# Optimization experiments

Measured on AMD Instinct MI355X. Metric: run time of the kernel, lower is better.

Reference implementation:

```python
import jax, jax.numpy as jnp
import numpy as np

DN = ('NCHW', 'OIHW', 'NCHW')
B, T, D, H, W = 8, 10, 10, 128, 128
WINDOW_OUT = 5


def conv2d(x, w, b):
    y = jax.lax.conv_general_dilated(x, w, (1, 1), 'SAME', dimension_numbers=DN)
    return y + b[None, :, None, None]


def lstm_cell(x, h, c, w, b):
    # ConvLSTM gate update: conv over [x; h], split into i,f,o,g
    z = conv2d(jnp.concatenate([x, h], axis=1), w, b)
    i, f, o, g = jnp.split(z, 4, axis=1)
    c2 = jax.nn.sigmoid(f) * c + jax.nn.sigmoid(i) * jnp.tanh(g)
    h2 = jax.nn.sigmoid(o) * jnp.tanh(c2)
    return h2, c2


def attn_score(x, h, c, w1, b1, w2, b2):
    # conv-MLP attention score over concat([x, h, c]) -> (b, H, W)
    z = jnp.concatenate([x, h, c], axis=1)
    return conv2d(jnp.tanh(conv2d(z, w1, b1)), w2, b2)[:, 0]


def setup_inputs():
    key = jax.random.key(0)
    ks = jax.random.split(key, 16)
    s = 0.05
    return {
        'x': jax.random.normal(ks[0], (B, T, D, H, W), jnp.float32),
        'h0': jnp.zeros((B, 1, H, W), jnp.float32),
        'c0': jnp.zeros((B, 1, H, W), jnp.float32),
        'h1': jnp.zeros((B, 64, H, W), jnp.float32),
        'c1': jnp.zeros((B, 64, H, W), jnp.float32),
        # encoder cells: layer0 (in 10, hid 1), layer1 (in 1, hid 64)
        'w_enc0': jax.random.normal(ks[1], (4, 11, 3, 3), jnp.float32) * s,
        'b_enc0': jax.random.normal(ks[2], (4,), jnp.float32) * s,
        'w_enc1': jax.random.normal(ks[3], (256, 65, 3, 3), jnp.float32) * s,
        'b_enc1': jax.random.normal(ks[4], (256,), jnp.float32) * s,
        # decoder cells: layer0 (in 1, hid 64), layer1 (in 64, hid 1)
        'w_dec0': jax.random.normal(ks[5], (256, 65, 3, 3), jnp.float32) * s,
        'b_dec0': jax.random.normal(ks[6], (256,), jnp.float32) * s,
        'w_dec1': jax.random.normal(ks[7], (4, 65, 3, 3), jnp.float32) * s,
        'b_dec1': jax.random.normal(ks[8], (4,), jnp.float32) * s,
        # input attention: in 10+2*1=12 -> 32 -> 1
        'wa1': jax.random.normal(ks[9], (32, 12, 3, 3), jnp.float32) * s,
        'ba1': jax.random.normal(ks[10], (32,), jnp.float32) * s,
        'wa2': jax.random.normal(ks[11], (1, 32, 3, 3), jnp.float32) * s,
        'ba2': jax.random.normal(ks[12], (1,), jnp.float32) * s,
        # temporal attention: in 1+2*64=129 -> 32 -> 1
        'wt1': jax.random.normal(ks[13], (32, 129, 3, 3), jnp.float32) * s,
        'bt1': jax.random.normal(ks[14], (32,), jnp.float32) * s,
        'wt2': jax.random.normal(ks[15], (1, 32, 3, 3), jnp.float32) * s,
        'bt2': jnp.zeros((1,), jnp.float32),
    }


def reference(x, h0, c0, h1, c1, w_enc0, b_enc0, w_enc1, b_enc1,
              w_dec0, b_dec0, w_dec1, b_dec1,
              wa1, ba1, wa2, ba2, wt1, bt1, wt2, bt2):
    def input_attn(xx, h, c):
        # per-feature score; vmap over feature dim k (axis 2 of x)
        score = jax.vmap(lambda xk: attn_score(xk, h, c, wa1, ba1, wa2, ba2),
                         in_axes=2, out_axes=1)(xx)          # (b, D, H, W)
        alpha = jax.nn.softmax(score, axis=1)
        return xx * alpha[:, None]                            # broadcast over time

    # ---- encoder layer 0: input attention re-weights x every step (compounding)
    def step0(carry, t):
        xx, h, c = carry
        xx = input_attn(xx, h, c)
        h, c = lstm_cell(xx[:, t], h, c, w_enc0, b_enc0)
        return (xx, h, c), (h, c)

    _, (hs0, cs0) = jax.lax.scan(step0, (x, h0, c0), jnp.arange(T))
    hs0 = jnp.moveaxis(hs0, 0, 1)   # (b, T, 1, H, W)
    cs0 = jnp.moveaxis(cs0, 0, 1)

    # ---- encoder layer 1
    def step1(carry, xt):
        h, c = lstm_cell(xt, carry[0], carry[1], w_enc1, b_enc1)
        return (h, c), (h, c)

    _, (hs1, cs1) = jax.lax.scan(step1, (h1, c1), jnp.moveaxis(hs0, 1, 0))
    hs1 = jnp.moveaxis(hs1, 0, 1)   # (b, T, 64, H, W)
    cs1 = jnp.moveaxis(cs1, 0, 1)

    def temporal_attn(y, hb, cb):
        score = jax.vmap(lambda ht, ct: attn_score(y, ht, ct, wt1, bt1, wt2, bt2),
                         in_axes=1, out_axes=1)(hb, cb)       # (b, T, H, W)
        beta = jax.nn.softmax(score, axis=1)
        return jnp.sum(hb * beta[:, :, None], axis=1), cb[:, -1]

    # ---- decoder: states reversed -> layer0 uses encoder layer1 states, etc.
    y0 = x[:, -1, 0][:, None]       # x[:, [-1], selected_dim] -> (b, 1, H, W)

    def dec_step(carry, _):
        y, hb0, cb0, hb1, cb1 = carry
        ht, ct = temporal_attn(y, hb0, cb0)
        ht, ct = lstm_cell(y, ht, ct, w_dec0, b_dec0)
        y = ht
        hb0 = jnp.concatenate([hb0[:, 1:], ht[:, None]], axis=1)
        cb0 = jnp.concatenate([cb0[:, 1:], ct[:, None]], axis=1)
        ht2, ct2 = lstm_cell(y, hb1[:, -1], cb1[:, -1], w_dec1, b_dec1)
        y = ht2
        hb1 = jnp.concatenate([hb1[:, 1:], ht2[:, None]], axis=1)
        cb1 = jnp.concatenate([cb1[:, 1:], ct2[:, None]], axis=1)
        return (y, hb0, cb0, hb1, cb1), y

    _, ys = jax.lax.scan(dec_step, (y0, hs1, cs1, hs0, cs0), None, length=WINDOW_OUT)
    return jnp.moveaxis(ys, 0, 1)   # (b, window_out, 1, H, W)
```

## Files before the change

kernel.cpp:

```cpp
#include <hip/hip_runtime.h>


#define PX 16384L
#define T_ 10
#define D_ 10

__device__ __forceinline__ float fast_tanh(float x) {
    const float e = __builtin_exp2f(x * 2.88539008f);
    return 1.f - 2.f * __builtin_amdgcn_rcpf(e + 1.f);
}
__device__ __forceinline__ float fast_sig(float x) {
    const float e = __builtin_exp2f(x * -1.44269504f);
    return __builtin_amdgcn_rcpf(e + 1.f);
}
__device__ __forceinline__ float fast_exp(float x) {
    return __builtin_exp2f(x * 1.44269504f);
}

__device__ __forceinline__ void lstm_dev(
    float* lds,
    int tile, int hcb, int b,
    const float* __restrict__ in0, long bs0,
    const float* __restrict__ in1,
    const float* __restrict__ w, const float* __restrict__ bias,
    const float* __restrict__ cprev,
    float* __restrict__ hout, float* __restrict__ cout_)
{
    const int tid = threadIdx.x;
    const int tx = tid & 31, r0 = (tid >> 5) << 1;
    const int tileX = (tile & 3) << 5, tileY = (tile >> 2) << 4;
    const int hc0 = hcb << 1;
    float acc[16];
#pragma unroll
    for (int j = 0; j < 16; j++) acc[j] = 0.f;

    int g0[3]; float m0[3];
#pragma unroll
    for (int i = 0; i < 3; i++) {
        const int lidx = tid + i * 256;
        const int r = lidx / 34, cc = lidx - r * 34;
        const int gy = tileY + r - 1, gx = tileX + cc - 1;
        const bool inb = (lidx < 612) && ((unsigned)gy < 128u) && ((unsigned)gx < 128u);
        g0[i] = inb ? gy * 128 + gx : 0;
        m0[i] = inb ? 1.f : 0.f;
    }

    for (int cb = 0; cb < 65; cb += 8) {
        const int cmax = min(8, 65 - cb);
        for (int cl = 0; cl < cmax; cl++) {
            const int ci = cb + cl;
            const float* p = (ci == 0) ? in0 + (long)b * bs0
                                       : in1 + ((long)b * 64 + (ci - 1)) * PX;
#pragma unroll
            for (int i = 0; i < 3; i++) {
                const int lidx = tid + i * 256;
                if (lidx < 612) lds[cl * 612 + lidx] = m0[i] * p[g0[i]];
            }
        }
        __syncthreads();
        for (int cl = 0; cl < cmax; cl++) {
            float win[4][3];
#pragma unroll
            for (int dy = 0; dy < 4; dy++)
#pragma unroll
                for (int dx = 0; dx < 3; dx++)
                    win[dy][dx] = lds[cl * 612 + (r0 + dy) * 34 + tx + dx];
            const int ci = cb + cl;
#pragma unroll
            for (int j = 0; j < 2; j++)
#pragma unroll
                for (int g = 0; g < 4; g++) {
                    const float* wp = w + ((long)(g * 64 + hc0 + j) * 65 + ci) * 9;
#pragma unroll
                    for (int rr = 0; rr < 2; rr++) {
                        float a = acc[(j * 4 + g) * 2 + rr];
#pragma unroll
                        for (int ky = 0; ky < 3; ky++)
#pragma unroll
                            for (int kx = 0; kx < 3; kx++)
                                a = fmaf(wp[ky * 3 + kx], win[rr + ky][kx], a);
                        acc[(j * 4 + g) * 2 + rr] = a;
                    }
                }
        }
        __syncthreads();
    }
#pragma unroll
    for (int j = 0; j < 2; j++) {
        const int hc = hc0 + j;
        const float bi = bias[hc], bf = bias[64 + hc];
        const float bo = bias[128 + hc], bg = bias[192 + hc];
#pragma unroll
        for (int rr = 0; rr < 2; rr++) {
            const long opix = (long)(tileY + r0 + rr) * 128 + tileX + tx;
            const float i_ = fast_sig(acc[(j * 4 + 0) * 2 + rr] + bi);
            const float f_ = fast_sig(acc[(j * 4 + 1) * 2 + rr] + bf);
            const float o_ = fast_sig(acc[(j * 4 + 2) * 2 + rr] + bo);
            const float g_ = fast_tanh(acc[(j * 4 + 3) * 2 + rr] + bg);
            const float cp = cprev[((long)b * 64 + hc) * PX + opix];
            const float c2 = f_ * cp + i_ * g_;
            const float h2 = o_ * fast_tanh(c2);
            hout[((long)b * 64 + hc) * PX + opix] = h2;
            cout_[((long)b * 64 + hc) * PX + opix] = c2;
        }
    }
}

__device__ __forceinline__ void zpart_dev(
    float* lds,
    int tile, int cob, int b,
    const float* __restrict__ hsrc, const float* __restrict__ csrc,
    const float* __restrict__ wt1, const float* __restrict__ bt1,
    float* __restrict__ zdst)
{
    const int tid = threadIdx.x;
    const int tx = tid & 15, ty = tid >> 4;
    const int tileX = (tile & 7) << 4, tileY = (tile >> 3) << 4;
    const int co0 = cob << 3;
    float acc[8];
#pragma unroll
    for (int j = 0; j < 8; j++) acc[j] = 0.f;

    int g0[2]; float m0[2];
#pragma unroll
    for (int i = 0; i < 2; i++) {
        const int lidx = tid + i * 256;
        const int r = lidx / 18, cc = lidx - r * 18;
        const int gy = tileY + r - 1, gx = tileX + cc - 1;
        const bool inb = (lidx < 324) && ((unsigned)gy < 128u) && ((unsigned)gx < 128u);
        g0[i] = inb ? gy * 128 + gx : 0;
        m0[i] = inb ? 1.f : 0.f;
    }

    for (int cb = 0; cb < 128; cb += 4) {
        for (int cl = 0; cl < 4; cl++) {
            const int ci = cb + cl;
            const float* p = (ci < 64) ? hsrc + ((long)b * 64 + ci) * PX
                                       : csrc + ((long)b * 64 + (ci - 64)) * PX;
#pragma unroll
            for (int i = 0; i < 2; i++) {
                const int lidx = tid + i * 256;
                if (lidx < 324) lds[cl * 324 + lidx] = m0[i] * p[g0[i]];
            }
        }
        __syncthreads();
        for (int cl = 0; cl < 4; cl++) {
            float r9[9];
#pragma unroll
            for (int dy = 0; dy < 3; dy++)
#pragma unroll
                for (int dx = 0; dx < 3; dx++)
                    r9[dy * 3 + dx] = lds[cl * 324 + (ty + dy) * 18 + tx + dx];
            const int ci = cb + cl;
#pragma unroll
            for (int j = 0; j < 8; j++) {
                const float* wp = wt1 + ((long)(co0 + j) * 129 + 1 + ci) * 9;
                float a = acc[j];
#pragma unroll
                for (int q = 0; q < 9; q++) a = fmaf(wp[q], r9[q], a);
                acc[j] = a;
            }
        }
        __syncthreads();
    }
    const long opix = (long)(tileY + ty) * 128 + tileX + tx;
#pragma unroll
    for (int j = 0; j < 8; j++)
        zdst[((long)b * 32 + co0 + j) * PX + opix] = acc[j] + bt1[co0 + j];
}

__global__ __launch_bounds__(256)
void lstm_merge_k(const float* __restrict__ in0, long bs0,
                  const float* __restrict__ in1,
                  const float* __restrict__ w, const float* __restrict__ bias,
                  const float* __restrict__ cprev,
                  float* __restrict__ hout, float* __restrict__ cout_,
                  const float* __restrict__ zh, const float* __restrict__ zc,
                  float* __restrict__ zdst,
                  const float* __restrict__ wt1, const float* __restrict__ bt1)
{
    __shared__ float lds[8 * 612];
    const int bid = blockIdx.x, b = blockIdx.z;
    if (bid < 1024) {
        lstm_dev(lds, bid & 31, bid >> 5, b, in0, bs0, in1, w, bias,
                 cprev, hout, cout_);
    } else {
        const int q = bid - 1024;
        zpart_dev(lds, q & 63, q >> 6, b, zh, zc, wt1, bt1, zdst);
    }
}

__global__ __launch_bounds__(256)
void zpart_k(const float* __restrict__ zh, const float* __restrict__ zc,
             float* __restrict__ zdst,
             const float* __restrict__ wt1, const float* __restrict__ bt1)
{
    __shared__ float lds[4 * 324];
    zpart_dev(lds, blockIdx.x, blockIdx.y, blockIdx.z, zh, zc, wt1, bt1, zdst);
}

__global__ __launch_bounds__(256)
void dec_merge_k(const float* __restrict__ hs1s,
                 const float* __restrict__ hb1, long hb1bs,
                 const float* __restrict__ w1,
                 float* __restrict__ l1p, int nbs,
                 const float* __restrict__ zc, float* __restrict__ zdst,
                 const float* __restrict__ wt1, const float* __restrict__ bt1)
{
    __shared__ float lds[4 * 324];
    const int bid = blockIdx.x, b = blockIdx.z;
    if (bid < 256) {
        const int tile = bid & 63, s = bid >> 6;
        const int ci0 = (s == 0) ? 0 : (s == 1) ? 17 : (s == 2) ? 33 : 49;
        const int cn  = (s == 0) ? 17 : 16;
        const int tid = threadIdx.x;
        const int tx = tid & 15, ty = tid >> 4;
        const int tileX = (tile & 7) << 4, tileY = (tile >> 3) << 4;
        int g0[2]; float m0[2];
#pragma unroll
        for (int i = 0; i < 2; i++) {
            const int lidx = tid + i * 256;
            const int r = lidx / 18, cc = lidx - r * 18;
            const int gy = tileY + r - 1, gx = tileX + cc - 1;
            const bool inb = (lidx < 324) && ((unsigned)gy < 128u) && ((unsigned)gx < 128u);
            g0[i] = inb ? gy * 128 + gx : 0;
            m0[i] = inb ? 1.f : 0.f;
        }
        float acc[4] = {0.f, 0.f, 0.f, 0.f};
        for (int cb = 0; cb < cn; cb += 4) {
            const int cmax = min(4, cn - cb);
            for (int cl = 0; cl < cmax; cl++) {
                const int ci = ci0 + cb + cl;
                const float* p = (ci < 64) ? hs1s + ((long)b * 64 + ci) * PX
                                           : hb1 + (long)b * hb1bs;
#pragma unroll
                for (int i = 0; i < 2; i++) {
                    const int lidx = tid + i * 256;
                    if (lidx < 324) lds[cl * 324 + lidx] = m0[i] * p[g0[i]];
                }
            }
            __syncthreads();
            for (int cl = 0; cl < cmax; cl++) {
                float r9[9];
#pragma unroll
                for (int dy = 0; dy < 3; dy++)
#pragma unroll
                    for (int dx = 0; dx < 3; dx++)
                        r9[dy * 3 + dx] = lds[cl * 324 + (ty + dy) * 18 + tx + dx];
                const int ci = ci0 + cb + cl;
#pragma unroll
                for (int j = 0; j < 4; j++) {
                    const float* wp = w1 + ((long)j * 65 + ci) * 9;
                    float a = acc[j];
#pragma unroll
                    for (int q = 0; q < 9; q++) a = fmaf(wp[q], r9[q], a);
                    acc[j] = a;
                }
            }
            __syncthreads();
        }
        const long opix = (long)(tileY + ty) * 128 + tileX + tx;
#pragma unroll
        for (int j = 0; j < 4; j++)
            l1p[(((long)s * nbs + b) * 4 + j) * PX + opix] = acc[j];
    } else {
        const int q = bid - 256;
        zpart_dev(lds, q & 63, q >> 6, b, hs1s, zc, wt1, bt1, zdst);
    }
}

__global__ __launch_bounds__(256)
void combine_lstm_k(const float* __restrict__ pbuf, int nsl, int hidden,
                    const float* __restrict__ bias,
                    const float* __restrict__ cprev, long cpbs,
                    float* __restrict__ hout, long hobs,
                    float* __restrict__ cout_, long cobs,
                    float* __restrict__ hout2, long ho2bs, int rb, int nbs)
{
    const long idx = (long)blockIdx.x * 256 + threadIdx.x;
    if (idx >= (long)rb * hidden * PX) return;
    const long px = idx & 16383;
    const long v = idx >> 14;
    const int hc = (int)(v % hidden), b = (int)(v / hidden);
    const int nco = 4 * hidden;
    float g4[4] = {0.f, 0.f, 0.f, 0.f};
    for (int s = 0; s < nsl; s++)
#pragma unroll
        for (int g = 0; g < 4; g++)
            g4[g] += pbuf[(((long)s * nbs + b) * nco + g * hidden + hc) * PX + px];
    const float i_ = fast_sig(g4[0] + bias[hc]);
    const float f_ = fast_sig(g4[1] + bias[hidden + hc]);
    const float o_ = fast_sig(g4[2] + bias[2 * hidden + hc]);
    const float g_ = fast_tanh(g4[3] + bias[3 * hidden + hc]);
    const float cp = cprev[(long)b * cpbs + (long)hc * PX + px];
    const float c2 = f_ * cp + i_ * g_;
    const float h2 = o_ * fast_tanh(c2);
    hout[(long)b * hobs + (long)hc * PX + px] = h2;
    cout_[(long)b * cobs + (long)hc * PX + px] = c2;
    if (hout2) hout2[(long)b * ho2bs + (long)hc * PX + px] = h2;
}

__global__ __launch_bounds__(256)
void enc0_lstm_k(const float* __restrict__ x, int t, const float* __restrict__ A,
                 const float* __restrict__ hprev, const float* __restrict__ cprev,
                 const float* __restrict__ w, const float* __restrict__ bias,
                 float* __restrict__ hout, float* __restrict__ cout_)
{
    __shared__ float lds[4 * 324];
    const int tid = threadIdx.x;
    const int tx = tid & 15, ty = tid >> 4;
    const int tile = blockIdx.x, b = blockIdx.z;
    const int tileX = (tile & 7) << 4, tileY = (tile >> 3) << 4;
    int g0[2]; float m0[2];
#pragma unroll
    for (int i = 0; i < 2; i++) {
        const int lidx = tid + i * 256;
        const int r = lidx / 18, cc = lidx - r * 18;
        const int gy = tileY + r - 1, gx = tileX + cc - 1;
        const bool inb = (lidx < 324) && ((unsigned)gy < 128u) && ((unsigned)gx < 128u);
        g0[i] = inb ? gy * 128 + gx : 0;
        m0[i] = inb ? 1.f : 0.f;
    }
    float acc[4] = {0.f, 0.f, 0.f, 0.f};
    for (int cb = 0; cb < 11; cb += 4) {
        const int cmax = min(4, 11 - cb);
        for (int cl = 0; cl < cmax; cl++) {
            const int ci = cb + cl;
#pragma unroll
            for (int i = 0; i < 2; i++) {
                const int lidx = tid + i * 256;
                if (lidx < 324) {
                    float v;
                    if (ci < 10) {
                        v = x[(((long)b * T_ + t) * D_ + ci) * PX + g0[i]]
                            * A[((long)b * 10 + ci) * PX + g0[i]];
                    } else {
                        v = hprev[(long)b * PX + g0[i]];
                    }
                    lds[cl * 324 + lidx] = m0[i] * v;
                }
            }
        }
        __syncthreads();
        for (int cl = 0; cl < cmax; cl++) {
            float r9[9];
#pragma unroll
            for (int dy = 0; dy < 3; dy++)
#pragma unroll
                for (int dx = 0; dx < 3; dx++)
                    r9[dy * 3 + dx] = lds[cl * 324 + (ty + dy) * 18 + tx + dx];
            const int ci = cb + cl;
#pragma unroll
            for (int g = 0; g < 4; g++) {
                const float* wp = w + ((long)g * 11 + ci) * 9;
                float a = acc[g];
#pragma unroll
                for (int q = 0; q < 9; q++) a = fmaf(wp[q], r9[q], a);
                acc[g] = a;
            }
        }
        __syncthreads();
    }
    const long opix = (long)(tileY + ty) * 128 + tileX + tx;
    const float i_ = fast_sig(acc[0] + bias[0]);
    const float f_ = fast_sig(acc[1] + bias[1]);
    const float o_ = fast_sig(acc[2] + bias[2]);
    const float g_ = fast_tanh(acc[3] + bias[3]);
    const float cp = cprev[(long)b * PX + opix];
    const float c2 = f_ * cp + i_ * g_;
    const float h2 = o_ * fast_tanh(c2);
    hout[(long)b * PX + opix] = h2;
    cout_[(long)b * PX + opix] = c2;
}

__global__ __launch_bounds__(256)
void iattn_k(const float* __restrict__ x, const float* __restrict__ A,
             const float* __restrict__ h, const float* __restrict__ c,
             const float* __restrict__ wa1, const float* __restrict__ ba1,
             const float* __restrict__ wa2, const float* __restrict__ ba2,
             float* __restrict__ score)
{
    __shared__ float xl[12][400];
    __shared__ float zl[8][324];
    const int tid = threadIdx.x;
    const int tileX = (blockIdx.x & 7) << 4, tileY = (blockIdx.x >> 3) << 4;
    const int z = blockIdx.z;
    const int b = z & 7, k = z >> 3;

    int g0[2]; float m0[2]; float aTr[2];
#pragma unroll
    for (int i = 0; i < 2; i++) {
        const int lidx = tid + i * 256;
        const int r = lidx / 20, cc = lidx - r * 20;
        const int gy = tileY + r - 2, gx = tileX + cc - 2;
        const bool inb = (lidx < 400) && ((unsigned)gy < 128u) && ((unsigned)gx < 128u);
        g0[i] = inb ? gy * 128 + gx : 0;
        m0[i] = inb ? 1.f : 0.f;
        aTr[i] = A ? (m0[i] * A[((long)b * 10 + k) * PX + g0[i]]) : 1.f;
    }
    for (int ch = 0; ch < 12; ch++) {
        const float* p = (ch < 10) ? x + (((long)b * 10 + ch) * 10 + k) * PX
                       : (ch == 10) ? h + (long)b * PX : c + (long)b * PX;
#pragma unroll
        for (int i = 0; i < 2; i++) {
            const int lidx = tid + i * 256;
            if (lidx < 400) {
                float v = m0[i] * p[g0[i]];
                if (ch < 10) v *= aTr[i];
                xl[ch][lidx] = v;
            }
        }
    }
    __syncthreads();

    const int i0 = tid;
    const int i1 = tid + 256;
    const int zr0 = i0 / 18, zc0 = i0 - zr0 * 18;
    const int zr1 = (i1 < 324) ? i1 / 18 : 0;
    const int zc1 = (i1 < 324) ? i1 - zr1 * 18 : 0;
    const int gy0 = tileY + zr0 - 1, gx0 = tileX + zc0 - 1;
    const bool in0_ = ((unsigned)gy0 < 128u) && ((unsigned)gx0 < 128u);
    const int gy1 = tileY + zr1 - 1, gx1 = tileX + zc1 - 1;
    const bool in1_ = (i1 < 324) && ((unsigned)gy1 < 128u) && ((unsigned)gx1 < 128u);

    const int tx = tid & 15, ty = tid >> 4;
    float sacc = ba2[0];

    for (int hf = 0; hf < 4; hf++) {
        float acc0[8], acc1[8];
#pragma unroll
        for (int co = 0; co < 8; co++) { acc0[co] = 0.f; acc1[co] = 0.f; }
        for (int ci = 0; ci < 12; ci++) {
            float wA[9], wB[9];
#pragma unroll
            for (int dy = 0; dy < 3; dy++)
#pragma unroll
                for (int dx = 0; dx < 3; dx++) {
                    wA[dy * 3 + dx] = xl[ci][(zr0 + dy) * 20 + zc0 + dx];
                    wB[dy * 3 + dx] = xl[ci][(zr1 + dy) * 20 + zc1 + dx];
                }
#pragma unroll
            for (int co = 0; co < 8; co++) {
                const float* wp = wa1 + ((long)(hf * 8 + co) * 12 + ci) * 9;
                float a0 = acc0[co], a1 = acc1[co];
#pragma unroll
                for (int q = 0; q < 9; q++) {
                    a0 = fmaf(wp[q], wA[q], a0);
                    a1 = fmaf(wp[q], wB[q], a1);
                }
                acc0[co] = a0; acc1[co] = a1;
            }
        }
        if (hf) __syncthreads();
#pragma unroll
        for (int co = 0; co < 8; co++) {
            zl[co][i0] = in0_ ? fast_tanh(acc0[co] + ba1[hf * 8 + co]) : 0.f;
            if (i1 < 324) zl[co][i1] = in1_ ? fast_tanh(acc1[co] + ba1[hf * 8 + co]) : 0.f;
        }
        __syncthreads();
        for (int co = 0; co < 8; co++) {
            const float* wp = wa2 + (hf * 8 + co) * 9;
#pragma unroll
            for (int ky = 0; ky < 3; ky++)
#pragma unroll
                for (int kx = 0; kx < 3; kx++)
                    sacc = fmaf(wp[ky * 3 + kx], zl[co][(ty + ky) * 18 + tx + kx], sacc);
        }
    }
    score[((long)b * 10 + k) * PX + (long)(tileY + ty) * 128 + tileX + tx] = sacc;
}

__global__ __launch_bounds__(256)
void softmax_mul_k(const float* __restrict__ s, float* __restrict__ A, int nb, int init)
{
    const long idx = (long)blockIdx.x * 256 + threadIdx.x;
    if (idx >= (long)nb * PX) return;
    const long b = idx >> 14, p = idx & 16383;
    const float* base = s + b * 10 * PX + p;
    float v[10]; float m = -1e30f;
#pragma unroll
    for (int t = 0; t < 10; t++) { v[t] = base[t * PX]; m = fmaxf(m, v[t]); }
    float sum = 0.f;
#pragma unroll
    for (int t = 0; t < 10; t++) { v[t] = fast_exp(v[t] - m); sum += v[t]; }
    const float r = __builtin_amdgcn_rcpf(sum);
    float* Ab = A + b * 10 * PX + p;
#pragma unroll
    for (int t = 0; t < 10; t++)
        Ab[t * PX] = init ? (v[t] * r) : (Ab[t * PX] * v[t] * r);
}

__global__ __launch_bounds__(256)
void attn_fuse_k(const float* __restrict__ y, long ybs,
                 const float* __restrict__ zpart,
                 const float* __restrict__ wt1,
                 const float* __restrict__ wt2, const float* __restrict__ bt2,
                 float* __restrict__ score, int rb, int nbs)
{
    __shared__ float ylds[400];
    __shared__ float zl[16][324];
    const int tid = threadIdx.x;
    const int tileX = (blockIdx.x & 7) << 4, tileY = (blockIdx.x >> 3) << 4;
    const int z = blockIdx.z;
    const int b = z % rb, t = z / rb;

#pragma unroll
    for (int i = 0; i < 2; i++) {
        const int lidx = tid + i * 256;
        if (lidx < 400) {
            const int r = lidx / 20, cc = lidx - r * 20;
            const int gy = tileY + r - 2, gx = tileX + cc - 2;
            const bool inb = ((unsigned)gy < 128u) && ((unsigned)gx < 128u);
            ylds[lidx] = inb ? y[(long)b * ybs + gy * 128 + gx] : 0.f;
        }
    }
    __syncthreads();

    const int i0 = tid, i1 = tid + 256;
    const int zr0 = i0 / 18, zc0 = i0 - zr0 * 18;
    const int zr1 = (i1 < 324) ? i1 / 18 : 0;
    const int zc1 = (i1 < 324) ? i1 - zr1 * 18 : 0;
    const int gy0 = tileY + zr0 - 1, gx0 = tileX + zc0 - 1;
    const bool in0_ = ((unsigned)gy0 < 128u) && ((unsigned)gx0 < 128u);
    const int gy1 = tileY + zr1 - 1, gx1 = tileX + zc1 - 1;
    const bool in1_ = (i1 < 324) && ((unsigned)gy1 < 128u) && ((unsigned)gx1 < 128u);
    const long pix0 = in0_ ? (long)gy0 * 128 + gx0 : 0;
    const long pix1 = in1_ ? (long)gy1 * 128 + gx1 : 0;
    const float* zp0 = zpart + ((long)t * nbs + b) * 32 * PX;

    const int tx = tid & 15, ty = tid >> 4;
    float sacc = bt2[0];

    for (int hf = 0; hf < 2; hf++) {
        float yw0[9], yw1[9];
#pragma unroll
        for (int dy = 0; dy < 3; dy++)
#pragma unroll
            for (int dx = 0; dx < 3; dx++) {
                yw0[dy * 3 + dx] = ylds[(zr0 + dy) * 20 + zc0 + dx];
                yw1[dy * 3 + dx] = ylds[(zr1 + dy) * 20 + zc1 + dx];
            }
        if (hf) __syncthreads();
#pragma unroll 4
        for (int ch = 0; ch < 16; ch++) {
            const int cg = hf * 16 + ch;
            const float* wy = wt1 + (long)cg * 129 * 9;
            float s0 = zp0[(long)cg * PX + pix0];
            float s1 = (i1 < 324) ? zp0[(long)cg * PX + pix1] : 0.f;
#pragma unroll
            for (int q = 0; q < 9; q++) {
                s0 = fmaf(wy[q], yw0[q], s0);
                s1 = fmaf(wy[q], yw1[q], s1);
            }
            zl[ch][i0] = in0_ ? fast_tanh(s0) : 0.f;
            if (i1 < 324) zl[ch][i1] = in1_ ? fast_tanh(s1) : 0.f;
        }
        __syncthreads();
        for (int ch = 0; ch < 16; ch++) {
            const float* wp = wt2 + (hf * 16 + ch) * 9;
#pragma unroll
            for (int ky = 0; ky < 3; ky++)
#pragma unroll
                for (int kx = 0; kx < 3; kx++)
                    sacc = fmaf(wp[ky * 3 + kx], zl[ch][(ty + ky) * 18 + tx + kx], sacc);
        }
    }
    score[((long)b * 10 + t) * PX + (long)(tileY + ty) * 128 + tileX + tx] = sacc;
}

__global__ __launch_bounds__(256)
void smax_wsum_k(const float* __restrict__ score, const float* __restrict__ hs1,
                 float* __restrict__ aht, int rb, int nbs)
{
    const long idx = (long)blockIdx.x * 256 + threadIdx.x;
    if (idx >= (long)rb * PX) return;
    const long b = idx >> 14, p = idx & 16383;
    const int ch0 = blockIdx.y * 8;
    const float* base = score + b * 10 * PX + p;
    float v[10]; float m = -1e30f;
#pragma unroll
    for (int t = 0; t < 10; t++) { v[t] = base[t * PX]; m = fmaxf(m, v[t]); }
    float sum = 0.f;
#pragma unroll
    for (int t = 0; t < 10; t++) { v[t] = fast_exp(v[t] - m); sum += v[t]; }
    const float r = __builtin_amdgcn_rcpf(sum);
#pragma unroll
    for (int t = 0; t < 10; t++) v[t] *= r;
    const long slot1 = (long)nbs * 64 * PX;
#pragma unroll
    for (int j = 0; j < 8; j++) {
        const int ch = ch0 + j;
        float a = 0.f;
#pragma unroll
        for (int t = 0; t < 10; t++)
            a += v[t] * hs1[t * slot1 + (b * 64 + ch) * PX + p];
        aht[(b * 64 + ch) * PX + p] = a;
    }
}

extern "C" void kernel_launch(void* const* d_in, const int* in_sizes, int n_in,
                              void* d_out, int out_size, void* d_ws, size_t ws_size,
                              hipStream_t stream)
{
    const float* x      = (const float*)d_in[0];
    const float* h0     = (const float*)d_in[1];
    const float* c0in   = (const float*)d_in[2];
    const float* h1     = (const float*)d_in[3];
    const float* c1     = (const float*)d_in[4];
    const float* w_enc0 = (const float*)d_in[5];
    const float* b_enc0 = (const float*)d_in[6];
    const float* w_enc1 = (const float*)d_in[7];
    const float* b_enc1 = (const float*)d_in[8];
    const float* w_dec0 = (const float*)d_in[9];
    const float* b_dec0 = (const float*)d_in[10];
    const float* w_dec1 = (const float*)d_in[11];
    const float* b_dec1 = (const float*)d_in[12];
    const float* wa1 = (const float*)d_in[13];
    const float* ba1 = (const float*)d_in[14];
    const float* wa2 = (const float*)d_in[15];
    const float* ba2 = (const float*)d_in[16];
    const float* wt1 = (const float*)d_in[17];
    const float* bt1 = (const float*)d_in[18];
    const float* wt2 = (const float*)d_in[19];
    const float* bt2 = (const float*)d_in[20];
    float* out = (float*)d_out;

    const int tiers[7] = {8, 6, 5, 4, 3, 2, 1};
    int nb = 0;
    for (int ti = 0; ti < 7; ti++) {
        const size_t need = (size_t)(160 + 1188 * tiers[ti]) * PX * sizeof(float);
        if (need <= ws_size) { nb = tiers[ti]; break; }
    }
    if (nb == 0) return;

    float* ws = (float*)d_ws;
    float* hs0 = ws;
    float* cs0 = hs0 + 80 * PX;
    float* G   = cs0 + 80 * PX;
    float* A    = G;
    float* sc1  = G + 80 * PX;
    const long slot1  = (long)nb * 64 * PX;
    float* hs1   = G;
    float* cs1   = hs1 + 10 * slot1;
    float* zpart = cs1 + 2 * slot1;
    float* aht   = zpart + (long)10 * nb * 32 * PX;
    float* l1p   = aht + (long)nb * 64 * PX;
    float* hs0g  = l1p + (long)4 * nb * 4 * PX;
    float* cs0g  = hs0g + (long)5 * nb * PX;
    float* scD   = cs0g + (long)5 * nb * PX;

    const dim3 blk(256);
    const long TDP = (long)T_ * D_ * PX;
    const long zslot = (long)nb * 32 * PX;

    for (int t = 0; t < 10; t++) {
        const float* hprev = (t == 0) ? h0 : hs0 + (long)(t - 1) * 8 * PX;
        const float* cprev = (t == 0) ? c0in : cs0 + (long)(t - 1) * 8 * PX;
        iattn_k<<<dim3(64, 1, 80), blk, 0, stream>>>(
            x, (t == 0) ? nullptr : A, hprev, cprev, wa1, ba1, wa2, ba2, sc1);
        softmax_mul_k<<<512, blk, 0, stream>>>(sc1, A, 8, t == 0);
        enc0_lstm_k<<<dim3(64, 1, 8), blk, 0, stream>>>(
            x, t, A, hprev, cprev, w_enc0, b_enc0,
            hs0 + (long)t * 8 * PX, cs0 + (long)t * 8 * PX);
    }

    for (int b0 = 0; b0 < 8; b0 += nb) {
        const int rb = (8 - b0 < nb) ? (8 - b0) : nb;
        const float* xb  = x + (long)b0 * TDP;
        float* outb = out + (long)b0 * 5 * PX;

        for (int t = 0; t < 10; t++) {
            const float* hprev = (t == 0) ? h1 + (long)b0 * 64 * PX
                                          : hs1 + (long)(t - 1) * slot1;
            const float* cprev = (t == 0) ? c1 + (long)b0 * 64 * PX
                                          : cs1 + (long)((t - 1) & 1) * slot1;
            const int gx = (t == 0) ? 1024 : 1280;
            lstm_merge_k<<<dim3(gx, 1, rb), blk, 0, stream>>>(
                hs0 + (long)t * 8 * PX + (long)b0 * PX, PX,
                hprev, w_enc1, b_enc1, cprev,
                hs1 + (long)t * slot1, cs1 + (long)(t & 1) * slot1,
                (t == 0) ? nullptr : hs1 + (long)(t - 1) * slot1,
                (t == 0) ? nullptr : cs1 + (long)((t - 1) & 1) * slot1,
                (t == 0) ? nullptr : zpart + (long)(t - 1) * zslot,
                wt1, bt1);
        }
        zpart_k<<<dim3(64, 4, rb), blk, 0, stream>>>(
            hs1 + 9L * slot1, cs1 + slot1, zpart + 9L * zslot, wt1, bt1);

        for (int s = 0; s < 5; s++) {
            const float* yptr; long ybs;
            if (s == 0) { yptr = xb + 9L * D_ * PX; ybs = TDP; }
            else        { yptr = hs0g + (long)(s - 1) * nb * PX; ybs = PX; }
            const float* hb1 = (s == 0) ? hs0 + 9L * 8 * PX + (long)b0 * PX
                                        : hs0g + (long)(s - 1) * nb * PX;
            const float* cb1 = (s == 0) ? cs0 + 9L * 8 * PX + (long)b0 * PX
                                        : cs0g + (long)(s - 1) * nb * PX;

            attn_fuse_k<<<dim3(64, 1, 10 * rb), blk, 0, stream>>>(
                yptr, ybs, zpart, wt1, wt2, bt2, scD, rb, nb);
            smax_wsum_k<<<dim3((int)(((long)rb * PX + 255) / 256), 8), blk, 0, stream>>>(
                scD, hs1, aht, rb, nb);

            lstm_merge_k<<<dim3(1024, 1, rb), blk, 0, stream>>>(
                yptr, ybs, aht, w_dec0, b_dec0,
                cs1 + (long)((s + 1) & 1) * slot1,
                hs1 + (long)s * slot1, cs1 + (long)(s & 1) * slot1,
                nullptr, nullptr, nullptr, wt1, bt1);

            const int gx2 = (s < 4) ? 512 : 256;
            dec_merge_k<<<dim3(gx2, 1, rb), blk, 0, stream>>>(
                hs1 + (long)s * slot1, hb1, PX, w_dec1, l1p, nb,
                cs1 + (long)(s & 1) * slot1, zpart + (long)s * zslot, wt1, bt1);
            combine_lstm_k<<<(int)(((long)rb * PX + 255) / 256), blk, 0, stream>>>(
                l1p, 4, 1, b_dec1, cb1, PX,
                hs0g + (long)s * nb * PX, PX,
                cs0g + (long)s * nb * PX, PX,
                outb + (long)s * PX, 5 * PX, rb, nb);
        }
    }
}
```

Measured before the change: 18.88 ms.

## Interleave encoder layer0 attention with layer1 LSTM in one fused launch

Rewrites the input-attention kernel to use 16x8 tiles (128 blocks per image) as a device function. When all 8 batches fit in the workspace, the layer-0 attention for step t+1 is merged into the same launch as the layer-1 LSTM for step t. The two recurrences then run concurrently instead of doing all layer-0 steps first. This fills the GPU with more independent blocks per launch and removes the serial layer-0 phase, at the cost of a larger kernel with more branches and smaller attention tiles that carry more halo overhead.

Result: no change. 19.07 ms (+1.0%).

```diff
diff --git a/kernel.cpp b/kernel.cpp
--- a/kernel.cpp
+++ b/kernel.cpp
@@ -169,25 +169,130 @@
         zdst[((long)b * 32 + co0 + j) * PX + opix] = acc[j] + bt1[co0 + j];
 }
 
-__global__ __launch_bounds__(256)
-void lstm_merge_k(const float* __restrict__ in0, long bs0,
-                  const float* __restrict__ in1,
-                  const float* __restrict__ w, const float* __restrict__ bias,
-                  const float* __restrict__ cprev,
-                  float* __restrict__ hout, float* __restrict__ cout_,
-                  const float* __restrict__ zh, const float* __restrict__ zc,
-                  float* __restrict__ zdst,
-                  const float* __restrict__ wt1, const float* __restrict__ bt1)
-{
-    __shared__ float lds[8 * 612];
+__device__ __forceinline__ void iattn8_dev(
+    float* lds, int tile, int b, int k,
+    const float* __restrict__ x, const float* __restrict__ A,
+    const float* __restrict__ h, const float* __restrict__ c,
+    const float* __restrict__ wa1, const float* __restrict__ ba1,
+    const float* __restrict__ wa2, const float* __restrict__ ba2,
+    float* __restrict__ score)
+{
+    float* xl = lds;
+    float* zl = lds + 2880;
+    const int tid = threadIdx.x;
+    const int tileX = (tile & 7) << 4;
+    const int tileY = (tile >> 3) << 3;
+
+    int g0 = 0; float m0 = 0.f; float aTr = 1.f;
+    if (tid < 240) {
+        const int r = tid / 20, cc = tid - r * 20;
+        const int gy = tileY + r - 2, gx = tileX + cc - 2;
+        const bool inb = ((unsigned)gy < 128u) && ((unsigned)gx < 128u);
+        g0 = inb ? gy * 128 + gx : 0;
+        m0 = inb ? 1.f : 0.f;
+        aTr = A ? (m0 * A[((long)b * 10 + k) * PX + g0]) : 1.f;
+        for (int ch = 0; ch < 12; ch++) {
+            const float* p = (ch < 10) ? x + (((long)b * 10 + ch) * 10 + k) * PX
+                           : (ch == 10) ? h + (long)b * PX : c + (long)b * PX;
+            float v = m0 * p[g0];
+            if (ch < 10) v *= aTr;
+            xl[ch * 240 + tid] = v;
+        }
+    }
+    __syncthreads();
+
+    const int zr = (tid < 180) ? tid / 18 : 0;
+    const int zc = (tid < 180) ? tid - zr * 18 : 0;
+    const int gy0 = tileY + zr - 1, gx0 = tileX + zc - 1;
+    const bool in0_ = (tid < 180) && ((unsigned)gy0 < 128u) && ((unsigned)gx0 < 128u);
+    const int tx = tid & 15, ty = tid >> 4;
+    float sacc = ba2[0];
+
+    for (int hf = 0; hf < 4; hf++) {
+        float acc0[8];
+#pragma unroll
+        for (int co = 0; co < 8; co++) acc0[co] = 0.f;
+        if (tid < 192) {
+            for (int ci = 0; ci < 12; ci++) {
+                float wA[9];
+#pragma unroll
+                for (int dy = 0; dy < 3; dy++)
+#pragma unroll
+                    for (int dx = 0; dx < 3; dx++)
+                        wA[dy * 3 + dx] = xl[ci * 240 + (zr + dy) * 20 + zc + dx];
+#pragma unroll
+                for (int co = 0; co < 8; co++) {
+                    const float* wp = wa1 + ((long)(hf * 8 + co) * 12 + ci) * 9;
+                    float a0 = acc0[co];
+#pragma unroll
+                    for (int q = 0; q < 9; q++) a0 = fmaf(wp[q], wA[q], a0);
+                    acc0[co] = a0;
+                }
+            }
+        }
+        if (hf) __syncthreads();
+        if (tid < 180) {
+#pragma unroll
+            for (int co = 0; co < 8; co++)
+                zl[co * 180 + tid] = in0_ ? fast_tanh(acc0[co] + ba1[hf * 8 + co]) : 0.f;
+        }
+        __syncthreads();
+        if (tid < 128) {
+            for (int co = 0; co < 8; co++) {
+                const float* wp = wa2 + (hf * 8 + co) * 9;
+#pragma unroll
+                for (int ky = 0; ky < 3; ky++)
+#pragma unroll
+                    for (int kx = 0; kx < 3; kx++)
+                        sacc = fmaf(wp[ky * 3 + kx], zl[co * 180 + (ty + ky) * 18 + tx + kx], sacc);
+            }
+        }
+    }
+    if (tid < 128)
+        score[((long)b * 10 + k) * PX + (long)(tileY + ty) * 128 + tileX + tx] = sacc;
+}
+
+__global__ __launch_bounds__(256)
+void mega_k(const float* __restrict__ in0, long bs0,
+            const float* __restrict__ in1,
+            const float* __restrict__ w, const float* __restrict__ bias,
+            const float* __restrict__ cprev,
+            float* __restrict__ hout, float* __restrict__ cout_,
+            const float* __restrict__ zh, const float* __restrict__ zc,
+            float* __restrict__ zdst,
+            const float* __restrict__ wt1, const float* __restrict__ bt1,
+            const float* __restrict__ xi, const float* __restrict__ Ai,
+            const float* __restrict__ hi, const float* __restrict__ ci,
+            const float* __restrict__ wa1, const float* __restrict__ ba1,
+            const float* __restrict__ wa2, const float* __restrict__ ba2,
+            float* __restrict__ score)
+{
+    __shared__ float lds[4896];
     const int bid = blockIdx.x, b = blockIdx.z;
     if (bid < 1024) {
         lstm_dev(lds, bid & 31, bid >> 5, b, in0, bs0, in1, w, bias,
                  cprev, hout, cout_);
-    } else {
+    } else if (zdst && bid < 1280) {
         const int q = bid - 1024;
         zpart_dev(lds, q & 63, q >> 6, b, zh, zc, wt1, bt1, zdst);
-    }
+    } else {
+        const int q = bid - (zdst ? 1280 : 1024);
+        iattn8_dev(lds, q & 127, b, q >> 7, xi, Ai, hi, ci,
+                   wa1, ba1, wa2, ba2, score);
+    }
+}
+
+__global__ __launch_bounds__(256)
+void iattn_k(const float* __restrict__ x, const float* __restrict__ A,
+             const float* __restrict__ h, const float* __restrict__ c,
+             const float* __restrict__ wa1, const float* __restrict__ ba1,
+             const float* __restrict__ wa2, const float* __restrict__ ba2,
+             float* __restrict__ score)
+{
+    __shared__ float lds[4320];
+    const int z = blockIdx.z;
+    iattn8_dev(lds, blockIdx.x, z & 7, z >> 3, x, A, h, c,
+               wa1, ba1, wa2, ba2, score);
 }
 
 __global__ __launch_bounds__(256)
@@ -371,103 +476,6 @@
     const float h2 = o_ * fast_tanh(c2);
     hout[(long)b * PX + opix] = h2;
     cout_[(long)b * PX + opix] = c2;
-}
-
-__global__ __launch_bounds__(256)
-void iattn_k(const float* __restrict__ x, const float* __restrict__ A,
-             const float* __restrict__ h, const float* __restrict__ c,
-             const float* __restrict__ wa1, const float* __restrict__ ba1,
-             const float* __restrict__ wa2, const float* __restrict__ ba2,
-             float* __restrict__ score)
-{
-    __shared__ float xl[12][400];
-    __shared__ float zl[8][324];
-    const int tid = threadIdx.x;
-    const int tileX = (blockIdx.x & 7) << 4, tileY = (blockIdx.x >> 3) << 4;
-    const int z = blockIdx.z;
-    const int b = z & 7, k = z >> 3;
-
-    int g0[2]; float m0[2]; float aTr[2];
-#pragma unroll
-    for (int i = 0; i < 2; i++) {
-        const int lidx = tid + i * 256;
-        const int r = lidx / 20, cc = lidx - r * 20;
-        const int gy = tileY + r - 2, gx = tileX + cc - 2;
-        const bool inb = (lidx < 400) && ((unsigned)gy < 128u) && ((unsigned)gx < 128u);
-        g0[i] = inb ? gy * 128 + gx : 0;
-        m0[i] = inb ? 1.f : 0.f;
-        aTr[i] = A ? (m0[i] * A[((long)b * 10 + k) * PX + g0[i]]) : 1.f;
-    }
-    for (int ch = 0; ch < 12; ch++) {
-        const float* p = (ch < 10) ? x + (((long)b * 10 + ch) * 10 + k) * PX
-                       : (ch == 10) ? h + (long)b * PX : c + (long)b * PX;
-#pragma unroll
-        for (int i = 0; i < 2; i++) {
-            const int lidx = tid + i * 256;
-            if (lidx < 400) {
-                float v = m0[i] * p[g0[i]];
-                if (ch < 10) v *= aTr[i];
-                xl[ch][lidx] = v;
-            }
-        }
-    }
-    __syncthreads();
-
-    const int i0 = tid;
-    const int i1 = tid + 256;
-    const int zr0 = i0 / 18, zc0 = i0 - zr0 * 18;
-    const int zr1 = (i1 < 324) ? i1 / 18 : 0;
-    const int zc1 = (i1 < 324) ? i1 - zr1 * 18 : 0;
-    const int gy0 = tileY + zr0 - 1, gx0 = tileX + zc0 - 1;
-    const bool in0_ = ((unsigned)gy0 < 128u) && ((unsigned)gx0 < 128u);
-    const int gy1 = tileY + zr1 - 1, gx1 = tileX + zc1 - 1;
-    const bool in1_ = (i1 < 324) && ((unsigned)gy1 < 128u) && ((unsigned)gx1 < 128u);
-
-    const int tx = tid & 15, ty = tid >> 4;
-    float sacc = ba2[0];
-
-    for (int hf = 0; hf < 4; hf++) {
-        float acc0[8], acc1[8];
-#pragma unroll
-        for (int co = 0; co < 8; co++) { acc0[co] = 0.f; acc1[co] = 0.f; }
-        for (int ci = 0; ci < 12; ci++) {
-            float wA[9], wB[9];
-#pragma unroll
-            for (int dy = 0; dy < 3; dy++)
-#pragma unroll
-                for (int dx = 0; dx < 3; dx++) {
-                    wA[dy * 3 + dx] = xl[ci][(zr0 + dy) * 20 + zc0 + dx];
-                    wB[dy * 3 + dx] = xl[ci][(zr1 + dy) * 20 + zc1 + dx];
-                }
-#pragma unroll
-            for (int co = 0; co < 8; co++) {
-                const float* wp = wa1 + ((long)(hf * 8 + co) * 12 + ci) * 9;
-                float a0 = acc0[co], a1 = acc1[co];
-#pragma unroll
-                for (int q = 0; q < 9; q++) {
-                    a0 = fmaf(wp[q], wA[q], a0);
-                    a1 = fmaf(wp[q], wB[q], a1);
-                }
-                acc0[co] = a0; acc1[co] = a1;
-            }
-        }
-        if (hf) __syncthreads();
-#pragma unroll
-        for (int co = 0; co < 8; co++) {
-            zl[co][i0] = in0_ ? fast_tanh(acc0[co] + ba1[hf * 8 + co]) : 0.f;
-            if (i1 < 324) zl[co][i1] = in1_ ? fast_tanh(acc1[co] + ba1[hf * 8 + co]) : 0.f;
-        }
-        __syncthreads();
-        for (int co = 0; co < 8; co++) {
-            const float* wp = wa2 + (hf * 8 + co) * 9;
-#pragma unroll
-            for (int ky = 0; ky < 3; ky++)
-#pragma unroll
-                for (int kx = 0; kx < 3; kx++)
-                    sacc = fmaf(wp[ky * 3 + kx], zl[co][(ty + ky) * 18 + tx + kx], sacc);
-        }
-    }
-    score[((long)b * 10 + k) * PX + (long)(tileY + ty) * 128 + tileX + tx] = sacc;
 }
 
 __global__ __launch_bounds__(256)
@@ -632,13 +640,12 @@
         if (need <= ws_size) { nb = tiers[ti]; break; }
     }
     if (nb == 0) return;
+    const bool ilv = (nb == 8);
 
     float* ws = (float*)d_ws;
     float* hs0 = ws;
     float* cs0 = hs0 + 80 * PX;
     float* G   = cs0 + 80 * PX;
-    float* A    = G;
-    float* sc1  = G + 80 * PX;
     const long slot1  = (long)nb * 64 * PX;
     float* hs1   = G;
     float* cs1   = hs1 + 10 * slot1;
@@ -648,20 +655,55 @@
     float* hs0g  = l1p + (long)4 * nb * 4 * PX;
     float* cs0g  = hs0g + (long)5 * nb * PX;
     float* scD   = cs0g + (long)5 * nb * PX;
+    float* A   = ilv ? aht : G;
+    float* sc1 = A + 80 * PX;
 
     const dim3 blk(256);
     const long TDP = (long)T_ * D_ * PX;
     const long zslot = (long)nb * 32 * PX;
 
-    for (int t = 0; t < 10; t++) {
-        const float* hprev = (t == 0) ? h0 : hs0 + (long)(t - 1) * 8 * PX;
-        const float* cprev = (t == 0) ? c0in : cs0 + (long)(t - 1) * 8 * PX;
-        iattn_k<<<dim3(64, 1, 80), blk, 0, stream>>>(
-            x, (t == 0) ? nullptr : A, hprev, cprev, wa1, ba1, wa2, ba2, sc1);
-        softmax_mul_k<<<512, blk, 0, stream>>>(sc1, A, 8, t == 0);
+    if (ilv) {
+        iattn_k<<<dim3(128, 1, 80), blk, 0, stream>>>(
+            x, nullptr, h0, c0in, wa1, ba1, wa2, ba2, sc1);
+        softmax_mul_k<<<512, blk, 0, stream>>>(sc1, A, 8, 1);
         enc0_lstm_k<<<dim3(64, 1, 8), blk, 0, stream>>>(
-            x, t, A, hprev, cprev, w_enc0, b_enc0,
-            hs0 + (long)t * 8 * PX, cs0 + (long)t * 8 * PX);
+            x, 0, A, h0, c0in, w_enc0, b_enc0, hs0, cs0);
+        for (int t = 0; t < 10; t++) {
+            const float* hprev1 = (t == 0) ? h1 : hs1 + (long)(t - 1) * slot1;
+            const float* cprev1 = (t == 0) ? c1 : cs1 + (long)((t - 1) & 1) * slot1;
+            const bool zp = (t > 0), ia = (t < 9);
+            const int gx = 1024 + (zp ? 256 : 0) + (ia ? 1280 : 0);
+            mega_k<<<dim3(gx, 1, 8), blk, 0, stream>>>(
+                hs0 + (long)t * 8 * PX, PX, hprev1, w_enc1, b_enc1, cprev1,
+                hs1 + (long)t * slot1, cs1 + (long)(t & 1) * slot1,
+                zp ? hs1 + (long)(t - 1) * slot1 : nullptr,
+                zp ? cs1 + (long)((t - 1) & 1) * slot1 : nullptr,
+                zp ? zpart + (long)(t - 1) * zslot : nullptr,
+                wt1, bt1,
+                x, A, hs0 + (long)t * 8 * PX, cs0 + (long)t * 8 * PX,
+                wa1, ba1, wa2, ba2, ia ? sc1 : nullptr);
+            if (ia) {
+                softmax_mul_k<<<512, blk, 0, stream>>>(sc1, A, 8, 0);
+                enc0_lstm_k<<<dim3(64, 1, 8), blk, 0, stream>>>(
+                    x, t + 1, A,
+                    hs0 + (long)t * 8 * PX, cs0 + (long)t * 8 * PX,
+                    w_enc0, b_enc0,
+                    hs0 + (long)(t + 1) * 8 * PX, cs0 + (long)(t + 1) * 8 * PX);
+            }
+        }
+        zpart_k<<<dim3(64, 4, 8), blk, 0, stream>>>(
+            hs1 + 9L * slot1, cs1 + slot1, zpart + 9L * zslot, wt1, bt1);
+    } else {
+        for (int t = 0; t < 10; t++) {
+            const float* hprev0 = (t == 0) ? h0 : hs0 + (long)(t - 1) * 8 * PX;
+            const float* cprev0 = (t == 0) ? c0in : cs0 + (long)(t - 1) * 8 * PX;
+            iattn_k<<<dim3(128, 1, 80), blk, 0, stream>>>(
+                x, (t == 0) ? nullptr : A, hprev0, cprev0, wa1, ba1, wa2, ba2, sc1);
+            softmax_mul_k<<<512, blk, 0, stream>>>(sc1, A, 8, t == 0);
+            enc0_lstm_k<<<dim3(64, 1, 8), blk, 0, stream>>>(
+                x, t, A, hprev0, cprev0, w_enc0, b_enc0,
+                hs0 + (long)t * 8 * PX, cs0 + (long)t * 8 * PX);
+        }
     }
 
     for (int b0 = 0; b0 < 8; b0 += nb) {
@@ -669,23 +711,27 @@
         const float* xb  = x + (long)b0 * TDP;
         float* outb = out + (long)b0 * 5 * PX;
 
-        for (int t = 0; t < 10; t++) {
-            const float* hprev = (t == 0) ? h1 + (long)b0 * 64 * PX
-                                          : hs1 + (long)(t - 1) * slot1;
-            const float* cprev = (t == 0) ? c1 + (long)b0 * 64 * PX
-                                          : cs1 + (long)((t - 1) & 1) * slot1;
-            const int gx = (t == 0) ? 1024 : 1280;
-            lstm_merge_k<<<dim3(gx, 1, rb), blk, 0, stream>>>(
-                hs0 + (long)t * 8 * PX + (long)b0 * PX, PX,
-                hprev, w_enc1, b_enc1, cprev,
-                hs1 + (long)t * slot1, cs1 + (long)(t & 1) * slot1,
-                (t == 0) ? nullptr : hs1 + (long)(t - 1) * slot1,
-                (t == 0) ? nullptr : cs1 + (long)((t - 1) & 1) * slot1,
-                (t == 0) ? nullptr : zpart + (long)(t - 1) * zslot,
-                wt1, bt1);
-        }
-        zpart_k<<<dim3(64, 4, rb), blk, 0, stream>>>(
-            hs1 + 9L * slot1, cs1 + slot1, zpart + 9L * zslot, wt1, bt1);
+        if (!ilv) {
+            for (int t = 0; t < 10; t++) {
+                const float* hprev = (t == 0) ? h1 + (long)b0 * 64 * PX
+                                              : hs1 + (long)(t - 1) * slot1;
+                const float* cprev = (t == 0) ? c1 + (long)b0 * 64 * PX
+                                              : cs1 + (long)((t - 1) & 1) * slot1;
+                const bool zp = (t > 0);
+                mega_k<<<dim3(zp ? 1280 : 1024, 1, rb), blk, 0, stream>>>(
+                    hs0 + (long)t * 8 * PX + (long)b0 * PX, PX,
+                    hprev, w_enc1, b_enc1, cprev,
+                    hs1 + (long)t * slot1, cs1 + (long)(t & 1) * slot1,
+                    zp ? hs1 + (long)(t - 1) * slot1 : nullptr,
+                    zp ? cs1 + (long)((t - 1) & 1) * slot1 : nullptr,
+                    zp ? zpart + (long)(t - 1) * zslot : nullptr,
+                    wt1, bt1,
+                    nullptr, nullptr, nullptr, nullptr,
+                    nullptr, nullptr, nullptr, nullptr, nullptr);
+            }
+            zpart_k<<<dim3(64, 4, rb), blk, 0, stream>>>(
+                hs1 + 9L * slot1, cs1 + slot1, zpart + 9L * zslot, wt1, bt1);
+        }
 
         for (int s = 0; s < 5; s++) {
             const float* yptr; long ybs;
@@ -701,11 +747,13 @@
             smax_wsum_k<<<dim3((int)(((long)rb * PX + 255) / 256), 8), blk, 0, stream>>>(
                 scD, hs1, aht, rb, nb);
 
-            lstm_merge_k<<<dim3(1024, 1, rb), blk, 0, stream>>>(
+            mega_k<<<dim3(1024, 1, rb), blk, 0, stream>>>(
                 yptr, ybs, aht, w_dec0, b_dec0,
                 cs1 + (long)((s + 1) & 1) * slot1,
                 hs1 + (long)s * slot1, cs1 + (long)(s & 1) * slot1,
-                nullptr, nullptr, nullptr, wt1, bt1);
+                nullptr, nullptr, nullptr, wt1, bt1,
+                nullptr, nullptr, nullptr, nullptr,
+                nullptr, nullptr, nullptr, nullptr, nullptr);
 
             const int gx2 = (s < 4) ? 512 : 256;
             dec_merge_k<<<dim3(gx2, 1, rb), blk, 0, stream>>>(
```
